# Kernel optimization log

Measured on AMD Instinct MI355X. Metric: run time of the kernel, lower is better.

The kernel has to match this reference:

```python
import jax, jax.numpy as jnp
import numpy as np

V, E, H, D = 50257, 512, 512, 2  # vocab, embed_dim, hidden_dim, depth (nlayers)
B, S, T = 32, 60, 48             # batch, encoder len, target len


def setup_inputs() -> dict:
    key = jax.random.key(0)
    ks = jax.random.split(key, 9)
    return {
        "enc_h": jax.random.normal(ks[0], (B, S, 2 * H), jnp.float32),
        "prev_s": jax.random.normal(ks[1], (B, H), jnp.float32),
        "target": jax.random.randint(ks[2], (T, B), 0, V),
        "embed_W": jax.random.normal(ks[3], (V, E), jnp.float32) * 0.02,
        "attn_W": jax.random.normal(ks[4], (2 * H, H), jnp.float32) * (1.0 / np.sqrt(2 * H)),
        "attn_b": jnp.zeros((H,), jnp.float32),
        "inp_W": jax.random.normal(ks[5], (E, 2 * H), jnp.float32) * (1.0 / np.sqrt(E)),
        "inp_b": jnp.zeros((2 * H,), jnp.float32),
        "cell_W": jax.random.normal(ks[6], (D, H, 2 * H), jnp.float32) * (1.0 / np.sqrt(H)),
        "cell_b": jnp.zeros((D, 2 * H), jnp.float32),
        "out_W": jax.random.normal(ks[7], (H, V), jnp.float32) * (1.0 / np.sqrt(H)),
        "out_b": jnp.zeros((V,), jnp.float32),
    }


def reference(enc_h, prev_s, target, embed_W, attn_W, attn_b,
              inp_W, inp_b, cell_W, cell_b, out_W, out_b):
    # target: T x B -> embeddings T x B x E
    emb = embed_W[target]
    # enc_h is fixed across timesteps: precompute attention keys (B x S x H)
    energy = jnp.tanh(enc_h @ attn_W + attn_b)
    depth = cell_W.shape[0]

    def step(s, x_t):
        # attention: scores B x S, ctx B x 2H
        scores = jnp.einsum("bsh,bh->bs", energy, s)
        alpha = jax.nn.softmax(scores, axis=-1)
        ctx = jnp.einsum("bs,bsd->bd", alpha, enc_h)
        ctx_e = ctx[:, :E]  # module uses ctx[:, 0:embed_dim] (j never updated)
        for l in range(depth):  # small fixed depth loop
            Ws = (s * ctx_e) @ cell_W[l] + cell_b[l]
            if l == 0:
                Ws = Ws + x_t @ inp_W + inp_b
            hh, tt = jnp.split(Ws, 2, axis=1)
            hh = jnp.tanh(hh)
            tt = jax.nn.sigmoid(tt)
            s = hh * tt + s * (1.0 - tt)  # highway gate (dropout p=0)
        return s, s

    _, dec_h = jax.lax.scan(step, prev_s, emb)  # T x B x H
    return dec_h @ out_W + out_b  # T x B x V
```

## Files before the change

### kernel.cpp

```cpp
#include <hip/hip_runtime.h>
#include <hip/hip_bf16.h>
#include <math.h>

#define B_ 32
#define S_ 60
#define T_ 48
#define H_ 512
#define E_ 512
#define V_ 50257
#define NPAD 50432
#define EPI_LD 260

typedef __attribute__((ext_vector_type(8))) short bf16x8v;
typedef __attribute__((ext_vector_type(4))) float f32x4v;
typedef __attribute__((ext_vector_type(4))) float f32x4a __attribute__((aligned(4)));
typedef __attribute__((ext_vector_type(4))) unsigned int u32x4;

__device__ inline unsigned short f2bf(float f) {
    union { float f; unsigned u; } v; v.f = f;
    unsigned r = v.u + 0x7fffu + ((v.u >> 16) & 1u);
    return (unsigned short)(r >> 16);
}
__device__ inline float bflo(unsigned u) { return __uint_as_float(u << 16); }

__device__ inline void gload_lds16(const void* g, void* l) {
    __builtin_amdgcn_global_load_lds(
        (const __attribute__((address_space(1))) unsigned int*)g,
        (__attribute__((address_space(3))) unsigned int*)l, 16, 0, 0);
}

__device__ __forceinline__ u32x4 ld_cohx4(const void* p) {
    u32x4 r;
    asm volatile("global_load_dwordx4 %0, %1, off sc0 sc1"
                 : "=v"(r) : "v"(p) : "memory");
    return r;
}
__device__ __forceinline__ float ld_coh_f32(const float* p) {
    float r;
    asm volatile("global_load_dword %0, %1, off sc0 sc1\n\ts_waitcnt vmcnt(0)"
                 : "=v"(r) : "v"(p) : "memory");
    return r;
}
__device__ __forceinline__ float ld_coh_f32_nw(const float* p) {
    float r;
    asm volatile("global_load_dword %0, %1, off sc0 sc1"
                 : "=v"(r) : "v"(p) : "memory");
    return r;
}
__device__ __forceinline__ void st_coh_f32(float* p, float v) {
    asm volatile("global_store_dword %0, %1, off sc0 sc1"
                 :: "v"(p), "v"(v) : "memory");
}
__device__ __forceinline__ void st_coh_u16(unsigned short* p, unsigned int v) {
    asm volatile("global_store_short %0, %1, off sc0 sc1"
                 :: "v"(p), "v"(v) : "memory");
}
__device__ __forceinline__ void st_coh_u32(int* p, int v) {
    asm volatile("global_store_dword %0, %1, off sc0 sc1"
                 :: "v"(p), "v"(v) : "memory");
}
__device__ __forceinline__ int ld_coh_u32(const int* p) {
    int r;
    asm volatile("global_load_dword %0, %1, off sc0 sc1\n\ts_waitcnt vmcnt(0)"
                 : "=v"(r) : "v"(p) : "memory");
    return r;
}

__device__ __forceinline__ void gbar(int* flags, int idx, int bi) {
    asm volatile("s_waitcnt vmcnt(0)" ::: "memory");
    __syncthreads();
    if (threadIdx.x == 0)
        st_coh_u32(&flags[idx * 32 + bi], 1);
    if (threadIdx.x < 64) {
        const int* fp = &flags[idx * 32 + (threadIdx.x & 31)];
        for (;;) {
            int v = ld_coh_u32(fp);
            if (__all(v != 0)) break;
            __builtin_amdgcn_s_sleep(1);
        }
    }
    __syncthreads();
}

template<int ACT, bool GATHER>
__device__ void gemm_body(const float* __restrict__ A, const float* __restrict__ Bm,
                          const float* __restrict__ bias, float* __restrict__ C,
                          int N, int K, int lda, const int* __restrict__ gidx,
                          int cb, int rb, float (*As)[128], float (*Bs)[128])
{
    const int tid = threadIdx.x;
    const int am = tid >> 1;
    const int ak = (tid & 1) * 4;
    const int arow = rb + am;
    const float* Arow;
    if (GATHER) Arow = A + (size_t)gidx[arow] * lda;
    else        Arow = A + (size_t)arow * lda;

    const int bk = tid >> 5;
    const int bn = (tid & 31) * 4;

    const int tx = tid & 15, ty = tid >> 4;
    float acc[8][8];
    #pragma unroll
    for (int i = 0; i < 8; i++)
        #pragma unroll
        for (int j = 0; j < 8; j++) acc[i][j] = 0.f;

    for (int k0 = 0; k0 < K; k0 += 8) {
        float4 av = *(const float4*)(Arow + k0 + ak);
        float4 bv = *(const float4*)(Bm + (size_t)(k0 + bk) * N + cb + bn);
        __syncthreads();
        As[ak + 0][am] = av.x; As[ak + 1][am] = av.y;
        As[ak + 2][am] = av.z; As[ak + 3][am] = av.w;
        Bs[bk][bn + 0] = bv.x; Bs[bk][bn + 1] = bv.y;
        Bs[bk][bn + 2] = bv.z; Bs[bk][bn + 3] = bv.w;
        __syncthreads();

        #pragma unroll
        for (int k = 0; k < 8; k++) {
            float a[8], b[8];
            *(float4*)(a)     = *(const float4*)&As[k][ty * 4];
            *(float4*)(a + 4) = *(const float4*)&As[k][ty * 4 + 64];
            *(float4*)(b)     = *(const float4*)&Bs[k][tx * 4];
            *(float4*)(b + 4) = *(const float4*)&Bs[k][tx * 4 + 64];
            #pragma unroll
            for (int i = 0; i < 8; i++)
                #pragma unroll
                for (int j = 0; j < 8; j++)
                    acc[i][j] = fmaf(a[i], b[j], acc[i][j]);
        }
    }

    #pragma unroll
    for (int i = 0; i < 8; i++) {
        int row = rb + ((i < 4) ? (ty * 4 + i) : (64 + ty * 4 + (i - 4)));
        #pragma unroll
        for (int j = 0; j < 8; j++) {
            int col = cb + ((j < 4) ? (tx * 4 + j) : (64 + tx * 4 + (j - 4)));
            float v = acc[i][j] + bias[col];
            if (ACT == 1) v = tanhf(v);
            C[(size_t)row * N + col] = v;
        }
    }
}

__global__ __launch_bounds__(256)
void gemm_pro(const float* __restrict__ enc_h, const float* __restrict__ attn_W,
              const float* __restrict__ attn_b, float* __restrict__ energy,
              const float* __restrict__ embed_W, const float* __restrict__ inp_W,
              const float* __restrict__ inp_b, float* __restrict__ pre,
              const int* __restrict__ target, int* __restrict__ cnt)
{
    __shared__ float As[8][128];
    __shared__ float Bs[8][128];
    const int bx = blockIdx.x;
    if (bx < 60) {
        const int cb = (bx & 3) * 128, rb = (bx >> 2) * 128;
        gemm_body<1, false>(enc_h, attn_W, attn_b, energy,
                            512, 1024, 1024, nullptr, cb, rb, As, Bs);
    } else if (bx < 156) {
        const int b2 = bx - 60;
        const int cb = (b2 & 7) * 128, rb = (b2 >> 3) * 128;
        gemm_body<0, true>(embed_W, inp_W, inp_b, pre,
                           1024, 512, 512, target, cb, rb, As, Bs);
    } else {
        for (int i = threadIdx.x; i < 144 * 32; i += 256) cnt[i] = 0;
    }
}

union __align__(16) ScanSM {
    struct {
        float eL[S_][H_];
        float part[8 * 32 * 36];
        float sCol[512];
    } s;
    float til[2 * 32 * 33];
};

template<int LI>
__device__ __forceinline__ void highway(
    int t, int bi, int tid, int lane, int wv,
    const bf16x8v (&wf)[2][2],
    const unsigned short* __restrict__ xsrc,
    unsigned short* __restrict__ xG1,
    const float* __restrict__ ctxG,
    float* __restrict__ sG,
    unsigned short* __restrict__ dec_b,
    const float* __restrict__ pre,
    float cbh, float cbt,
    float* part, float* sCol)
{
    const int l15 = lane & 15, lc = lane >> 4;
    const int b = tid >> 4, hi = tid & 15;
    const int h = bi * 16 + hi;

    float cxv = 0.f, prh = 0.f, prt = 0.f;
    if (LI == 0) {
        cxv = ld_coh_f32_nw(ctxG + (size_t)b * 512 + h);
        const float* pr = pre + ((size_t)t * B_ + b) * 1024;
        prh = pr[h]; prt = pr[h + 512];
    }

    u32x4 xr[2][2][2];
    #pragma unroll
    for (int ktl = 0; ktl < 2; ++ktl)
        #pragma unroll
        for (int pl = 0; pl < 2; ++pl)
            #pragma unroll
            for (int mt = 0; mt < 2; ++mt) {
                int ch = (((wv * 2 + ktl) * 2 + pl) * 4 + lc) * 32 + mt * 16 + l15;
                xr[ktl][pl][mt] = ld_cohx4(xsrc + (size_t)ch * 8);
            }
    asm volatile("s_waitcnt vmcnt(0)" ::: "memory");
    __builtin_amdgcn_sched_barrier(0);

    f32x4v acc[2][2];
    #pragma unroll
    for (int mt = 0; mt < 2; ++mt)
        #pragma unroll
        for (int nt = 0; nt < 2; ++nt) acc[mt][nt] = (f32x4v)0.f;

    #pragma unroll
    for (int ktl = 0; ktl < 2; ++ktl)
        #pragma unroll
        for (int pl = 0; pl < 2; ++pl)
            #pragma unroll
            for (int mt = 0; mt < 2; ++mt) {
                bf16x8v xv = *(bf16x8v*)&xr[ktl][pl][mt];
                #pragma unroll
                for (int nt = 0; nt < 2; ++nt)
                    acc[mt][nt] = __builtin_amdgcn_mfma_f32_16x16x32_bf16(
                        wf[ktl][nt], xv, acc[mt][nt], 0, 0, 0);
            }

    #pragma unroll
    for (int mt = 0; mt < 2; ++mt)
        #pragma unroll
        for (int nt = 0; nt < 2; ++nt)
            *(f32x4v*)&part[(wv * 32 + mt * 16 + l15) * 36 + nt * 16 + lc * 4] = acc[mt][nt];
    __syncthreads();

    float rh = 0.f, rt = 0.f;
    #pragma unroll
    for (int w = 0; w < 8; ++w) {
        rh += part[(w * 32 + b) * 36 + hi];
        rt += part[(w * 32 + b) * 36 + 16 + hi];
    }
    float ph = rh + cbh, pt = rt + cbt;
    if (LI == 0) { ph += prh; pt += prt; }
    float hh = tanhf(ph);
    float tg = 1.f / (1.f + __expf(-pt));
    float sold = sCol[tid];
    float sn = hh * tg + sold * (1.f - tg);
    sCol[tid] = sn;
    if (LI == 0) {
        float x1 = sn * cxv;
        unsigned short xh = f2bf(x1);
        unsigned short xl = f2bf(x1 - bflo((unsigned)xh));
        int kt = h >> 5, lc2 = (h >> 3) & 3, jj = h & 7;
        int ch = (kt * 8 + lc2) * 32 + b;
        st_coh_u16(xG1 + (size_t)ch * 8 + jj, xh);
        st_coh_u16(xG1 + (size_t)(ch + 128) * 8 + jj, xl);
    } else {
        st_coh_f32(sG + ((size_t)bi * 32 + b) * 16 + hi, sn);
        dec_b[((size_t)bi * 1536 + (size_t)t * B_ + b) * 16 + hi] = f2bf(sn);
    }
}

__global__ __launch_bounds__(512, 2)
void scan_tr(const float* __restrict__ energy, const float* __restrict__ enc_h,
             const float* __restrict__ prev_s, const float* __restrict__ pre,
             const float* __restrict__ cell_W, const float* __restrict__ cell_b,
             unsigned short* __restrict__ dec_b,
             const float* __restrict__ outW, unsigned short* __restrict__ Wt,
             float* __restrict__ ctxG, float* __restrict__ sG,
             unsigned short* __restrict__ xG0, unsigned short* __restrict__ xG1,
             int* __restrict__ cnt)
{
    __shared__ ScanSM sm;
    const int tid = threadIdx.x;

    if (blockIdx.x >= B_) {
        const int hb = blockIdx.x - B_;
        const int g = tid >> 8;
        const int tt0 = tid & 255;
        const int r = tt0 >> 3, c4 = (tt0 & 7) * 4;
        float* til = sm.til;
        #pragma unroll 1
        for (int j = 0; j < 57; ++j) {
            const int tt = hb * 2 + g + j * 448;
            const bool act = tt < (NPAD / 32) * 16;
            int n0 = 0, k0 = 0;
            if (act) {
                n0 = (tt >> 4) * 32;
                k0 = (tt & 15) * 32;
                #pragma unroll
                for (int jj = 0; jj < 4; ++jj) {
                    int n = n0 + c4 + jj;
                    til[(g * 32 + r) * 33 + c4 + jj] =
                        (n < V_) ? __builtin_nontemporal_load(&outW[(size_t)(k0 + r) * V_ + n]) : 0.f;
                }
            }
            __syncthreads();
            if (act) {
                const int n = n0 + r;
                unsigned lo = (unsigned)f2bf(til[(g * 32 + c4 + 0) * 33 + r])
                            | ((unsigned)f2bf(til[(g * 32 + c4 + 1) * 33 + r]) << 16);
                unsigned hi2 = (unsigned)f2bf(til[(g * 32 + c4 + 2) * 33 + r])
                             | ((unsigned)f2bf(til[(g * 32 + c4 + 3) * 33 + r]) << 16);
                unsigned long long ov = (unsigned long long)lo | ((unsigned long long)hi2 << 32);
                __builtin_nontemporal_store(ov, (unsigned long long*)&Wt[(size_t)n * 512 + k0 + c4]);
            }
            __syncthreads();
        }
        return;
    }

    const int bi = blockIdx.x;
    const int lane = tid & 63, wv = tid >> 6;
    float (*eL)[H_] = sm.s.eL;
    float* part   = sm.s.part;
    float* sA     = part;
    float* scoreL = part + 512;
    float* alphaL = part + 576;
    float* sCol   = sm.s.sCol;

    for (int i = tid; i < S_ * H_ / 4; i += 512) {
        int s = i >> 7, h4 = (i & 127) * 4;
        *(float4*)&eL[s][h4] = *(const float4*)&energy[((size_t)bi * S_ + s) * 512 + h4];
    }

    bf16x8v wf0[2][2], wf1[2][2];
    {
        const int l15 = lane & 15, lc = lane >> 4;
        #pragma unroll
        for (int ktl = 0; ktl < 2; ++ktl)
            #pragma unroll
            for (int nt = 0; nt < 2; ++nt) {
                const int kb = (wv * 2 + ktl) * 32 + lc * 8;
                const int n  = nt * 512 + bi * 16 + l15;
                #pragma unroll
                for (int jj = 0; jj < 8; ++jj) {
                    wf0[ktl][nt][jj] = (short)f2bf(cell_W[((size_t)(kb + jj)) * 1024 + n]);
                    wf1[ktl][nt][jj] = (short)f2bf(cell_W[((size_t)(512 + kb + jj)) * 1024 + n]);
                }
            }
    }
    const int hME = bi * 16 + (tid & 15);
    sCol[tid] = prev_s[(size_t)(tid >> 4) * 512 + hME];
    const float cb0h = cell_b[hME],        cb0t = cell_b[512 + hME];
    const float cb1h = cell_b[1024 + hME], cb1t = cell_b[1536 + hME];

    #pragma unroll 1
    for (int t = 0; t < T_; ++t) {
        float sAv;
        if (t == 0) sAv = prev_s[(size_t)bi * 512 + tid];
        else        sAv = ld_coh_f32(sG + ((size_t)(tid >> 4) * 32 + bi) * 16 + (tid & 15));
        __syncthreads();
        sA[tid] = sAv;
        __syncthreads();

        #pragma unroll 1
        for (int sp = 0; sp < 4; ++sp) {
            const int s0 = wv + sp * 16;
            const int s1 = s0 + 8;
            const bool has1 = (sp < 3) | (wv < 4);
            const float* e0 = &eL[s0][lane];
            const float* e1 = &eL[has1 ? s1 : s0][lane];
            float a0 = 0.f, a1 = 0.f;
            #pragma unroll
            for (int j = 0; j < 8; ++j) {
                float sv = sA[lane + j * 64];
                a0 = fmaf(e0[j * 64], sv, a0);
                a1 = fmaf(e1[j * 64], sv, a1);
            }
            #pragma unroll
            for (int off = 32; off; off >>= 1) {
                a0 += __shfl_xor(a0, off, 64);
                a1 += __shfl_xor(a1, off, 64);
            }
            if (lane == 0) {
                scoreL[s0] = a0;
                if (has1) scoreL[s1] = a1;
            }
        }
        __syncthreads();
        if (wv == 0) {
            float v = (lane < S_) ? scoreL[lane] : -3.4e38f;
            float m = v;
            #pragma unroll
            for (int off = 32; off; off >>= 1) m = fmaxf(m, __shfl_xor(m, off, 64));
            float e = (lane < S_) ? __expf(v - m) : 0.f;
            float su = e;
            #pragma unroll
            for (int off = 32; off; off >>= 1) su += __shfl_xor(su, off, 64);
            if (lane < S_) alphaL[lane] = e / su;
        }
        __syncthreads();
        {
            float a = 0.f;
            const float* ep = enc_h + (size_t)bi * S_ * 1024 + tid;
            #pragma unroll 20
            for (int s = 0; s < S_; ++s) a = fmaf(alphaL[s], ep[(size_t)s * 1024], a);
            st_coh_f32(ctxG + (size_t)bi * 512 + tid, a);
            float x0 = a * sA[tid];
            unsigned short xh = f2bf(x0);
            unsigned short xl = f2bf(x0 - bflo((unsigned)xh));
            int kt = tid >> 5, lc2 = (tid >> 3) & 3, jj = tid & 7;
            int ch = (kt * 8 + lc2) * 32 + bi;
            st_coh_u16(xG0 + (size_t)ch * 8 + jj, xh);
            st_coh_u16(xG0 + (size_t)(ch + 128) * 8 + jj, xl);
        }
        gbar(cnt, 3 * t + 0, bi);
        highway<0>(t, bi, tid, lane, wv, wf0, xG0, xG1, ctxG, sG, dec_b, pre,
                   cb0h, cb0t, part, sCol);
        gbar(cnt, 3 * t + 1, bi);
        highway<1>(t, bi, tid, lane, wv, wf1, xG1, xG1, ctxG, sG, dec_b, pre,
                   cb1h, cb1t, part, sCol);
        if (t != T_ - 1) gbar(cnt, 3 * t + 2, bi);
    }
}

__global__ __launch_bounds__(512)
void gemm_out(const unsigned short* __restrict__ dec, const unsigned short* __restrict__ Wt,
              const float* __restrict__ bias, float* __restrict__ out)
{
    __shared__ char smem[49152];
    short* As_wt  = (short*)smem;
    short* Bs_dec = (short*)(smem + 32768);
    float* epi    = (float*)smem;

    const int tid = threadIdx.x;
    const int lane = tid & 63, w = tid >> 6;
    const int wm = w >> 2, wn = w & 3;

    const int nwg = (NPAD / 256) * 12;
    const int qx = nwg >> 3, rx = nwg & 7;
    const int xcd = blockIdx.x & 7, idx = blockIdx.x >> 3;
    const int wgid = (xcd < rx ? xcd * (qx + 1) : rx * (qx + 1) + (xcd - rx) * qx) + idx;
    const int rb = (wgid % 12) * 128;
    const int cb = (wgid / 12) * 256;

#define STAGE_TILE(bi, kt) do {                                               \
        short* Ab_ = As_wt + (bi) * 8192;                                     \
        short* Bb_ = Bs_dec + (bi) * 4096;                                    \
        _Pragma("unroll")                                                     \
        for (int j_ = 0; j_ < 2; ++j_) {                                      \
            int rg_ = w * 2 + j_;                                             \
            int row_ = rg_ * 16 + (lane >> 2);                                \
            int kc_ = (lane & 3) ^ (row_ & 3);                                \
            gload_lds16(Wt + ((size_t)(cb + row_) * 512 + (kt) * 32 + kc_ * 8), \
                        Ab_ + rg_ * 512);                                     \
        }                                                                     \
        {                                                                     \
            int row_ = w * 16 + (lane >> 2);                                  \
            int kc_ = (lane & 3) ^ (row_ & 3);                                \
            gload_lds16(dec + (((size_t)((kt) * 2 + (kc_ >> 1)) * 1536 + (rb + row_)) * 16 \
                               + (kc_ & 1) * 8),                              \
                        Bb_ + w * 512);                                       \
        }                                                                     \
    } while (0)

    f32x4v acc[4][4];
    #pragma unroll
    for (int i = 0; i < 4; ++i)
        #pragma unroll
        for (int j = 0; j < 4; ++j) acc[i][j] = (f32x4v)0.f;

    STAGE_TILE(0, 0);

    #pragma unroll 1
    for (int it = 0; it < 16; ++it) {
        const int cur = it & 1;
        __builtin_amdgcn_s_barrier();
        asm volatile("" ::: "memory");
        if (it < 15) {
            STAGE_TILE(cur ^ 1, it + 1);
            asm volatile("s_waitcnt vmcnt(3)" ::: "memory");
        } else {
            asm volatile("s_waitcnt vmcnt(0)" ::: "memory");
        }
        __builtin_amdgcn_s_barrier();
        asm volatile("" ::: "memory");

        const short* Ab = As_wt + cur * 8192;
        const short* Bb = Bs_dec + cur * 4096;
        bf16x8v af[4], bf[4];
        const int lc = lane >> 4;
        #pragma unroll
        for (int ni = 0; ni < 4; ++ni) {
            int r = wn * 64 + ni * 16 + (lane & 15);
            af[ni] = *(const bf16x8v*)&Ab[r * 32 + ((lc ^ (r & 3)) * 8)];
        }
        #pragma unroll
        for (int mi = 0; mi < 4; ++mi) {
            int r = wm * 64 + mi * 16 + (lane & 15);
            bf[mi] = *(const bf16x8v*)&Bb[r * 32 + ((lc ^ (r & 3)) * 8)];
        }
        #pragma unroll
        for (int mi = 0; mi < 4; ++mi)
            #pragma unroll
            for (int ni = 0; ni < 4; ++ni)
                acc[mi][ni] = __builtin_amdgcn_mfma_f32_16x16x32_bf16(
                    af[ni], bf[mi], acc[mi][ni], 0, 0, 0);
    }
#undef STAGE_TILE

    const int c4 = (tid & 63) * 4;
    const bool fullcols = (cb + 256 <= V_);
    f32x4v bq = (f32x4v)0.f;
    if (fullcols) {
        float4 t4 = *(const float4*)(bias + cb + c4);
        bq[0] = t4.x; bq[1] = t4.y; bq[2] = t4.z; bq[3] = t4.w;
    }

    #pragma unroll
    for (int mi = 0; mi < 4; ++mi) {
        __syncthreads();
        #pragma unroll
        for (int ni = 0; ni < 4; ++ni) {
            const int er = wm * 16 + (lane & 15);
            const int ec = wn * 64 + ni * 16 + (lane >> 4) * 4;
            *(f32x4v*)&epi[er * EPI_LD + ec] = acc[mi][ni];
        }
        __syncthreads();
        #pragma unroll
        for (int j = 0; j < 4; ++j) {
            const int rr = w + j * 8;
            const int orow = rb + (rr >> 4) * 64 + mi * 16 + (rr & 15);
            f32x4v v = *(const f32x4v*)&epi[rr * EPI_LD + c4];
            if (fullcols) {
                v += bq;
                *(f32x4a*)(out + (size_t)orow * V_ + cb + c4) = v;
            } else {
                #pragma unroll
                for (int vv = 0; vv < 4; ++vv) {
                    const int col = cb + c4 + vv;
                    if (col < V_)
                        out[(size_t)orow * V_ + col] = v[vv] + bias[col];
                }
            }
        }
    }
}

extern "C" void kernel_launch(void* const* d_in, const int* in_sizes, int n_in,
                              void* d_out, int out_size, void* d_ws, size_t ws_size,
                              hipStream_t stream)
{
    const float* enc_h   = (const float*)d_in[0];
    const float* prev_s  = (const float*)d_in[1];
    const int*   target  = (const int*)  d_in[2];
    const float* embed_W = (const float*)d_in[3];
    const float* attn_W  = (const float*)d_in[4];
    const float* attn_b  = (const float*)d_in[5];
    const float* inp_W   = (const float*)d_in[6];
    const float* inp_b   = (const float*)d_in[7];
    const float* cell_W  = (const float*)d_in[8];
    const float* cell_b  = (const float*)d_in[9];
    const float* out_W   = (const float*)d_in[10];
    const float* out_b   = (const float*)d_in[11];
    float* out = (float*)d_out;

    float* ws = (float*)d_ws;
    float* energy = ws;
    float* pre    = energy + (size_t)B_ * S_ * H_;
    float* ctxG   = pre + (size_t)T_ * B_ * 2 * H_;
    float* sG     = ctxG + (size_t)B_ * H_;
    int*   cnt    = (int*)(sG + (size_t)B_ * H_);
    unsigned short* dec_b = (unsigned short*)(cnt + 144 * 32);
    unsigned short* xG0   = dec_b + (size_t)T_ * B_ * H_;
    unsigned short* xG1   = xG0 + (size_t)2 * B_ * H_;
    unsigned short* Wt    = xG1 + (size_t)2 * B_ * H_;

    gemm_pro<<<157, 256, 0, stream>>>(enc_h, attn_W, attn_b, energy,
                                      embed_W, inp_W, inp_b, pre, target, cnt);

    scan_tr<<<256, 512, 0, stream>>>(energy, enc_h, prev_s, pre, cell_W, cell_b,
                                     dec_b, out_W, Wt, ctxG, sG, xG0, xG1, cnt);

    gemm_out<<<(NPAD / 256) * 12, 512, 0, stream>>>(dec_b, Wt, out_b, out);
}
```

Before: 896.0 us.

## Replace third grid barrier per step with step-tagged state words polled by consumers

```diff
diff --git a/kernel.cpp b/kernel.cpp
--- a/kernel.cpp
+++ b/kernel.cpp
@@ -35,12 +35,6 @@
                  : "=v"(r) : "v"(p) : "memory");
     return r;
 }
-__device__ __forceinline__ float ld_coh_f32(const float* p) {
-    float r;
-    asm volatile("global_load_dword %0, %1, off sc0 sc1\n\ts_waitcnt vmcnt(0)"
-                 : "=v"(r) : "v"(p) : "memory");
-    return r;
-}
 __device__ __forceinline__ float ld_coh_f32_nw(const float* p) {
     float r;
     asm volatile("global_load_dword %0, %1, off sc0 sc1"
@@ -62,6 +56,16 @@
 __device__ __forceinline__ int ld_coh_u32(const int* p) {
     int r;
     asm volatile("global_load_dword %0, %1, off sc0 sc1\n\ts_waitcnt vmcnt(0)"
+                 : "=v"(r) : "v"(p) : "memory");
+    return r;
+}
+__device__ __forceinline__ void st_coh_u64(unsigned long long* p, unsigned long long v) {
+    asm volatile("global_store_dwordx2 %0, %1, off sc0 sc1"
+                 :: "v"(p), "v"(v) : "memory");
+}
+__device__ __forceinline__ unsigned long long ld_coh_u64(const unsigned long long* p) {
+    unsigned long long r;
+    asm volatile("global_load_dwordx2 %0, %1, off sc0 sc1\n\ts_waitcnt vmcnt(0)"
                  : "=v"(r) : "v"(p) : "memory");
     return r;
 }
@@ -149,7 +153,8 @@
               const float* __restrict__ attn_b, float* __restrict__ energy,
               const float* __restrict__ embed_W, const float* __restrict__ inp_W,
               const float* __restrict__ inp_b, float* __restrict__ pre,
-              const int* __restrict__ target, int* __restrict__ cnt)
+              const int* __restrict__ target, int* __restrict__ cnt,
+              unsigned long long* __restrict__ sG3)
 {
     __shared__ float As[8][128];
     __shared__ float Bs[8][128];
@@ -165,6 +170,7 @@
                            1024, 512, 512, target, cb, rb, As, Bs);
     } else {
         for (int i = threadIdx.x; i < 144 * 32; i += 256) cnt[i] = 0;
+        for (int i = threadIdx.x; i < 32 * 32 * 16; i += 256) sG3[i] = 0ull;
     }
 }
 
@@ -184,7 +190,7 @@
     const unsigned short* __restrict__ xsrc,
     unsigned short* __restrict__ xG1,
     const float* __restrict__ ctxG,
-    float* __restrict__ sG,
+    unsigned long long* __restrict__ sG3,
     unsigned short* __restrict__ dec_b,
     const float* __restrict__ pre,
     float cbh, float cbt,
@@ -262,7 +268,9 @@
         st_coh_u16(xG1 + (size_t)ch * 8 + jj, xh);
         st_coh_u16(xG1 + (size_t)(ch + 128) * 8 + jj, xl);
     } else {
-        st_coh_f32(sG + ((size_t)bi * 32 + b) * 16 + hi, sn);
+        unsigned long long q = (unsigned long long)__float_as_uint(sn)
+                             | ((unsigned long long)(unsigned)(t + 1) << 32);
+        st_coh_u64(sG3 + ((size_t)bi * 32 + b) * 16 + hi, q);
         dec_b[((size_t)bi * 1536 + (size_t)t * B_ + b) * 16 + hi] = f2bf(sn);
     }
 }
@@ -273,7 +281,7 @@
              const float* __restrict__ cell_W, const float* __restrict__ cell_b,
              unsigned short* __restrict__ dec_b,
              const float* __restrict__ outW, unsigned short* __restrict__ Wt,
-             float* __restrict__ ctxG, float* __restrict__ sG,
+             float* __restrict__ ctxG, unsigned long long* __restrict__ sG3,
              unsigned short* __restrict__ xG0, unsigned short* __restrict__ xG1,
              int* __restrict__ cnt)
 {
@@ -354,8 +362,19 @@
     #pragma unroll 1
     for (int t = 0; t < T_; ++t) {
         float sAv;
-        if (t == 0) sAv = prev_s[(size_t)bi * 512 + tid];
-        else        sAv = ld_coh_f32(sG + ((size_t)(tid >> 4) * 32 + bi) * 16 + (tid & 15));
+        if (t == 0) {
+            sAv = prev_s[(size_t)bi * 512 + tid];
+        } else {
+            const unsigned long long* sp =
+                sG3 + ((size_t)(tid >> 4) * 32 + bi) * 16 + (tid & 15);
+            unsigned long long q;
+            for (;;) {
+                q = ld_coh_u64(sp);
+                if (__all((int)(unsigned)(q >> 32) == t)) break;
+                __builtin_amdgcn_s_sleep(1);
+            }
+            sAv = __uint_as_float((unsigned)q);
+        }
         __syncthreads();
         sA[tid] = sAv;
         __syncthreads();
@@ -400,7 +419,7 @@
         {
             float a = 0.f;
             const float* ep = enc_h + (size_t)bi * S_ * 1024 + tid;
-            #pragma unroll 20
+            #pragma unroll
             for (int s = 0; s < S_; ++s) a = fmaf(alphaL[s], ep[(size_t)s * 1024], a);
             st_coh_f32(ctxG + (size_t)bi * 512 + tid, a);
             float x0 = a * sA[tid];
@@ -411,13 +430,12 @@
             st_coh_u16(xG0 + (size_t)ch * 8 + jj, xh);
             st_coh_u16(xG0 + (size_t)(ch + 128) * 8 + jj, xl);
         }
-        gbar(cnt, 3 * t + 0, bi);
-        highway<0>(t, bi, tid, lane, wv, wf0, xG0, xG1, ctxG, sG, dec_b, pre,
+        gbar(cnt, 2 * t + 0, bi);
+        highway<0>(t, bi, tid, lane, wv, wf0, xG0, xG1, ctxG, sG3, dec_b, pre,
                    cb0h, cb0t, part, sCol);
-        gbar(cnt, 3 * t + 1, bi);
-        highway<1>(t, bi, tid, lane, wv, wf1, xG1, xG1, ctxG, sG, dec_b, pre,
+        gbar(cnt, 2 * t + 1, bi);
+        highway<1>(t, bi, tid, lane, wv, wf1, xG1, xG1, ctxG, sG3, dec_b, pre,
                    cb1h, cb1t, part, sCol);
-        if (t != T_ - 1) gbar(cnt, 3 * t + 2, bi);
     }
 }
 
@@ -566,18 +584,18 @@
     float* energy = ws;
     float* pre    = energy + (size_t)B_ * S_ * H_;
     float* ctxG   = pre + (size_t)T_ * B_ * 2 * H_;
-    float* sG     = ctxG + (size_t)B_ * H_;
-    int*   cnt    = (int*)(sG + (size_t)B_ * H_);
+    unsigned long long* sG3 = (unsigned long long*)(ctxG + (size_t)B_ * H_);
+    int*   cnt    = (int*)(sG3 + (size_t)32 * 32 * 16);
     unsigned short* dec_b = (unsigned short*)(cnt + 144 * 32);
     unsigned short* xG0   = dec_b + (size_t)T_ * B_ * H_;
     unsigned short* xG1   = xG0 + (size_t)2 * B_ * H_;
     unsigned short* Wt    = xG1 + (size_t)2 * B_ * H_;
 
     gemm_pro<<<157, 256, 0, stream>>>(enc_h, attn_W, attn_b, energy,
-                                      embed_W, inp_W, inp_b, pre, target, cnt);
+                                      embed_W, inp_W, inp_b, pre, target, cnt, sG3);
 
     scan_tr<<<256, 512, 0, stream>>>(energy, enc_h, prev_s, pre, cell_W, cell_b,
-                                     dec_b, out_W, Wt, ctxG, sG, xG0, xG1, cnt);
+                                     dec_b, out_W, Wt, ctxG, sG3, xG0, xG1, cnt);
 
     gemm_out<<<(NPAD / 256) * 12, 512, 0, stream>>>(dec_b, Wt, out_b, out);
 }
```

New measurement: 1.143 ms. 27.5% more time.
